# Performance work log

Measured on AMD Instinct MI355X. Metric: run time of the kernel, lower is better.

Reference implementation:

```python
import jax, jax.numpy as jnp
import numpy as np

NUM_BINS = 36
MIN_ACTIVATION = 0.1
PENALTY_WEIGHT = 1.0


def setup_inputs() -> dict:
    key = jax.random.key(0)
    k1, k2 = jax.random.split(key)
    mask = jax.random.uniform(k1, (64, 1, 640, 640), dtype=jnp.float32)
    bbox = jax.random.uniform(k2, (64, 4), dtype=jnp.float32)
    return {"mask": mask, "bbox": bbox}


def reference(mask, bbox):
    B, _, H, W = mask.shape
    nb = NUM_BINS
    # pixel-space bbox centers
    cx = bbox[:, 0] * W  # (B,)
    cy = bbox[:, 1] * H  # (B,)
    x = jnp.arange(W, dtype=jnp.float32)
    y = jnp.arange(H, dtype=jnp.float32)
    # (B, H, W) offsets from each sample's center
    dx = x[None, None, :] - cx[:, None, None]
    dy = y[None, :, None] - cy[:, None, None]
    angles = jnp.arctan2(dy, dx)  # (B, H, W) in [-pi, pi]
    binf = (angles + jnp.pi) / (2.0 * jnp.pi) * nb
    bins = jnp.clip(binf.astype(jnp.int32), 0, nb - 1)  # (B, H, W)
    # fused per-(sample, bin) segment mean via a single scatter-add pass
    seg = (bins + jnp.arange(B, dtype=jnp.int32)[:, None, None] * nb).reshape(-1)
    m = mask[:, 0].reshape(-1)
    sums = jax.ops.segment_sum(m, seg, num_segments=B * nb)
    cnts = jax.ops.segment_sum(jnp.ones_like(m), seg, num_segments=B * nb)
    act = jnp.where(cnts > 0, sums / jnp.maximum(cnts, 1.0), 0.0).reshape(B, nb)
    under = (act < MIN_ACTIVATION).astype(jnp.float32)
    penalty_per_sample = under.sum(axis=1) / nb
    return PENALTY_WEIGHT * penalty_per_sample.mean()
```

## Files before the change

### kernel.cpp

```cpp
#include <hip/hip_runtime.h>
#include <math.h>

#define NB 36
#define W 640
#define H 640
#define NSAMP 64
#define RPB 40
#define BPS 16
#define NBLK (NSAMP * BPS)
#define FIX_SCALE 4194304.0f
#define INV_FIX (1.0f/4194304.0f)
#define CNT_SHIFT 44
#define SUM_MASK ((1ull << CNT_SHIFT) - 1)
#define AMB 1e-6

__device__ __constant__ double COT[36] = {
    0.0,
    5.6712818196177095,  2.7474774194546223,  1.7320508075688773,
    1.1917535925942100,  0.8390996311772800,  0.5773502691896258,
    0.3639702342662024,  0.1763269807084650,  0.0,
    -0.1763269807084650, -0.3639702342662024, -0.5773502691896258,
    -0.8390996311772800, -1.1917535925942100, -1.7320508075688773,
    -2.7474774194546223, -5.6712818196177095,
    0.0,
    5.6712818196177095,  2.7474774194546223,  1.7320508075688773,
    1.1917535925942100,  0.8390996311772800,  0.5773502691896258,
    0.3639702342662024,  0.1763269807084650,  0.0,
    -0.1763269807084650, -0.3639702342662024, -0.5773502691896258,
    -0.8390996311772800, -1.1917535925942100, -1.7320508075688773,
    -2.7474774194546223, -5.6712818196177095
};

__device__ __forceinline__ int bin_slow(int x, int y, double cxd, double cyd) {
    const double PI_D    = 3.141592653589793;
    const double TWOPI_D = 6.283185307179586;
    double t  = (atan2((double)y - cyd, (double)x - cxd) + PI_D) / TWOPI_D;
    double bd = t * 36.0;
    int k = (int)bd;
    k = k < 0 ? 0 : k;
    return k > NB - 1 ? NB - 1 : k;
}

#define SCAN_STEP(x, ctrl, rmask)                                             \
    x += (unsigned)__builtin_amdgcn_update_dpp(0, (int)(x), (ctrl), (rmask),  \
                                               0xf, false)

__global__ __launch_bounds__(256) void acl_main(const float* __restrict__ mask,
                                                const float* __restrict__ bbox,
                                                unsigned long long* __restrict__ ws) {
    __shared__ int A_l[RPB][18];
    __shared__ int sgn_l[RPB];
    __shared__ __align__(16) unsigned srow[4][768];
    __shared__ unsigned long long lbin[NB];

    const int tid = threadIdx.x;
    const int b   = blockIdx.x >> 4;
    const int rg  = blockIdx.x & (BPS - 1);
    const int y0  = rg * RPB;

    if (tid < NB) lbin[tid] = 0ull;
    if (tid < RPB) A_l[tid][17] = W - 1;

    const double cxd = (double)bbox[b * 4 + 0] * 640.0;
    const double cyd = (double)bbox[b * 4 + 1] * 640.0;

    for (int task = tid; task < RPB * 17; task += 256) {
        const int rl = task / 17, mi = task % 17;
        const int y  = y0 + rl;
        const double dy = (double)y - cyd;
        int i, a;
        if (dy == 0.0) {
            if (mi == 0) sgn_l[rl] = 0;
            i = mi;
            a = (mi == 0) ? ((int)ceil(cxd) - 1) : (W - 1);
        } else {
            const bool dp = (dy > 0.0);
            if (mi == 0) sgn_l[rl] = dp ? 1 : -1;
            const int m = dp ? (19 + mi) : (1 + mi);
            double x = cxd + dy * COT[m];
            x = fmin(fmax(x, -2.0), 642.0);
            double g  = x + 2.0;
            int    gi = (int)g;
            double fr = g - (double)gi;
            int v = dp ? (gi - 2)
                       : (gi - 1);
            if (fr < AMB || fr > 1.0 - AMB) {
                int xa = (int)(x + 2.5) - 2;
                if (xa >= 0 && xa <= W - 1) {
                    int kb = bin_slow(xa, y, cxd, cyd);
                    if (dp) v = (kb >= m) ? xa : xa - 1;
                    else    v = (kb >= m) ? xa : xa + 1;
                }
            }
            if (dp) { i = 16 - mi; a = v; }
            else    { i = mi;      a = v - 1; }
        }
        a = a < -1 ? -1 : (a > W - 1 ? W - 1 : a);
        A_l[rl][i] = a;
    }
    __syncthreads();

    const int wid = tid >> 6, lane = tid & 63;
    const float* rowbase = mask + (size_t)b * (W * H) + (size_t)y0 * W;

    unsigned long long accPs = 0ull, accNs = 0ull;
    unsigned accPc = 0u, accNc = 0u;

    const float4 z4 = make_float4(0.f, 0.f, 0.f, 0.f);
    const float4* rpA = (const float4*)(rowbase + (size_t)wid * W);
    float4 a0 = rpA[lane], a1 = rpA[lane + 64];
    float4 a2 = (lane < 32) ? rpA[lane + 128] : z4;
    const float4* rpB = (const float4*)(rowbase + (size_t)(wid + 4) * W);
    float4 b0 = rpB[lane], b1 = rpB[lane + 64];
    float4 b2 = (lane < 32) ? rpB[lane + 128] : z4;

    for (int j = 0; j < 10; j++) {
        const int rl = wid + 4 * j;
        float4 n0 = z4, n1 = z4, n2 = z4;
        if (j < 8) {
            const float4* np = (const float4*)(rowbase + (size_t)(rl + 8) * W);
            n0 = np[lane];
            n1 = np[lane + 64];
            n2 = (lane < 32) ? np[lane + 128] : z4;
        }

        unsigned carry = 0u;
        #pragma unroll
        for (int s = 0; s < 3; s++) {
            const float4 v = (s == 0) ? a0 : (s == 1) ? a1 : a2;
            const unsigned q0 = __float2uint_rn(v.x * FIX_SCALE);
            const unsigned q1 = __float2uint_rn(v.y * FIX_SCALE);
            const unsigned q2 = __float2uint_rn(v.z * FIX_SCALE);
            const unsigned q3 = __float2uint_rn(v.w * FIX_SCALE);
            const unsigned p0 = q0, p1 = p0 + q1, p2 = p1 + q2, p3 = p2 + q3;

            unsigned x = p3;
            SCAN_STEP(x, 0x111, 0xf);
            SCAN_STEP(x, 0x112, 0xf);
            SCAN_STEP(x, 0x114, 0xf);
            SCAN_STEP(x, 0x118, 0xf);
            SCAN_STEP(x, 0x142, 0xa);
            SCAN_STEP(x, 0x143, 0xc);
            const unsigned base = carry + (x - p3);
            uint4 wv;
            wv.x = base + p0; wv.y = base + p1; wv.z = base + p2; wv.w = base + p3;
            *((uint4*)&srow[wid][s * 256 + lane * 4]) = wv;
            carry += (unsigned)__builtin_amdgcn_readlane((int)x, 63);
        }

        if (lane < 18) {
            const int aR = A_l[rl][lane];
            const int aL = (lane == 0) ? -1 : A_l[rl][lane - 1];
            const int cnt = aR - aL;
            if (cnt > 0) {
                const unsigned sR = srow[wid][aR];
                const unsigned sL = (aL >= 0) ? srow[wid][aL] : 0u;
                const unsigned seg = sR - sL;
                const int sg = sgn_l[rl];
                if (sg > 0)      { accPc += (unsigned)cnt; accPs += seg; }
                else if (sg < 0) { accNc += (unsigned)cnt; accNs += seg; }
                else atomicAdd(&lbin[(lane == 0) ? 35 : 18],
                               ((unsigned long long)cnt << CNT_SHIFT)
                               + (unsigned long long)seg);
            }
        }
        a0 = b0; a1 = b1; a2 = b2;
        b0 = n0; b1 = n1; b2 = n2;
    }

    if (lane < 18) {
        if (accPc) atomicAdd(&lbin[35 - lane],
                             ((unsigned long long)accPc << CNT_SHIFT) + accPs);
        if (accNc) atomicAdd(&lbin[lane],
                             ((unsigned long long)accNc << CNT_SHIFT) + accNs);
    }
    __syncthreads();
    if (tid < NB)
        ws[(size_t)tid * NBLK + blockIdx.x] = lbin[tid];
}

__global__ __launch_bounds__(256) void acl_final(const unsigned long long* __restrict__ ws,
                                                 float* __restrict__ out) {
    __shared__ unsigned nund[256];
    __shared__ float s[NSAMP];
    const int tid = threadIdx.x;
    const int b = tid & 63, q = tid >> 6;
    unsigned cu = 0;
    #pragma unroll
    for (int kk = 0; kk < 9; kk++) {
        const int k = q * 9 + kk;
        const unsigned long long* base = ws + (size_t)k * NBLK + (size_t)b * BPS;
        unsigned long long t0 = 0ull, t1 = 0ull;
        #pragma unroll
        for (int g = 0; g < BPS; g += 2) {
            t0 += base[g];
            t1 += base[g + 1];
        }
        const unsigned long long tot = t0 + t1;
        const unsigned long long cnt = tot >> CNT_SHIFT;
        const float sum = (float)(tot & SUM_MASK) * INV_FIX;
        const float act = (cnt != 0ull) ? (sum / (float)cnt) : 0.0f;
        if (act < 0.1f) cu++;
    }
    nund[tid] = cu;
    __syncthreads();
    if (tid < NSAMP) {
        const unsigned n = nund[tid] + nund[64 + tid] + nund[128 + tid] + nund[192 + tid];
        s[tid] = (float)n / 36.0f;
    }
    __syncthreads();
    if (tid == 0) {
        float acc = 0.0f;
        for (int i = 0; i < NSAMP; i++) acc += s[i];
        out[0] = acc / 64.0f;
    }
}

extern "C" void kernel_launch(void* const* d_in, const int* in_sizes, int n_in,
                              void* d_out, int out_size, void* d_ws, size_t ws_size,
                              hipStream_t stream) {
    const float* mask = (const float*)d_in[0];
    const float* bbox = (const float*)d_in[1];
    unsigned long long* ws = (unsigned long long*)d_ws;

    acl_main<<<dim3(NBLK), dim3(256), 0, stream>>>(mask, bbox, ws);
    acl_final<<<dim3(1), dim3(256), 0, stream>>>(ws, (float*)d_out);
}
```

Baseline: 34.24 us.

## Issue first row loads before boundary setup and process two rows per iteration

New measurement: 34.44 us. Within noise of the previous version (+0.6%).

```diff
diff --git a/kernel.cpp b/kernel.cpp
--- a/kernel.cpp
+++ b/kernel.cpp
@@ -50,7 +50,7 @@
                                                 unsigned long long* __restrict__ ws) {
     __shared__ int A_l[RPB][18];
     __shared__ int sgn_l[RPB];
-    __shared__ __align__(16) unsigned srow[4][768];
+    __shared__ __align__(16) unsigned srow[8][768];
     __shared__ unsigned long long lbin[NB];
 
     const int tid = threadIdx.x;
@@ -60,6 +60,16 @@
 
     if (tid < NB) lbin[tid] = 0ull;
     if (tid < RPB) A_l[tid][17] = W - 1;
+
+    const int wid = tid >> 6, lane = tid & 63;
+    const float* wb = mask + (size_t)b * (W * H) + (size_t)(y0 + wid * 10) * W;
+    const float4 z4 = make_float4(0.f, 0.f, 0.f, 0.f);
+    const float4* pr0 = (const float4*)wb;
+    const float4* pr1 = (const float4*)(wb + W);
+    float4 cA0 = pr0[lane], cA1 = pr0[lane + 64];
+    float4 cA2 = (lane < 32) ? pr0[lane + 128] : z4;
+    float4 cB0 = pr1[lane], cB1 = pr1[lane + 64];
+    float4 cB2 = (lane < 32) ? pr1[lane + 128] : z4;
 
     const double cxd = (double)bbox[b * 4 + 0] * 640.0;
     const double cyd = (double)bbox[b * 4 + 1] * 640.0;
@@ -100,72 +110,81 @@
     }
     __syncthreads();
 
-    const int wid = tid >> 6, lane = tid & 63;
-    const float* rowbase = mask + (size_t)b * (W * H) + (size_t)y0 * W;
-
     unsigned long long accPs = 0ull, accNs = 0ull;
     unsigned accPc = 0u, accNc = 0u;
 
-    const float4 z4 = make_float4(0.f, 0.f, 0.f, 0.f);
-    const float4* rpA = (const float4*)(rowbase + (size_t)wid * W);
-    float4 a0 = rpA[lane], a1 = rpA[lane + 64];
-    float4 a2 = (lane < 32) ? rpA[lane + 128] : z4;
-    const float4* rpB = (const float4*)(rowbase + (size_t)(wid + 4) * W);
-    float4 b0 = rpB[lane], b1 = rpB[lane + 64];
-    float4 b2 = (lane < 32) ? rpB[lane + 128] : z4;
-
-    for (int j = 0; j < 10; j++) {
-        const int rl = wid + 4 * j;
-        float4 n0 = z4, n1 = z4, n2 = z4;
-        if (j < 8) {
-            const float4* np = (const float4*)(rowbase + (size_t)(rl + 8) * W);
-            n0 = np[lane];
-            n1 = np[lane + 64];
-            n2 = (lane < 32) ? np[lane + 128] : z4;
-        }
-
-        unsigned carry = 0u;
+    for (int j = 0; j < 5; j++) {
+        const int rl0 = wid * 10 + 2 * j;
+        float4 nA0, nA1, nA2, nB0, nB1, nB2;
+        if (j < 4) {
+            const float4* q0 = (const float4*)(wb + (size_t)(2 * j + 2) * W);
+            const float4* q1 = (const float4*)(wb + (size_t)(2 * j + 3) * W);
+            nA0 = q0[lane]; nA1 = q0[lane + 64];
+            nA2 = (lane < 32) ? q0[lane + 128] : z4;
+            nB0 = q1[lane]; nB1 = q1[lane + 64];
+            nB2 = (lane < 32) ? q1[lane + 128] : z4;
+        }
+
+        unsigned carryA = 0u, carryB = 0u;
         #pragma unroll
         for (int s = 0; s < 3; s++) {
-            const float4 v = (s == 0) ? a0 : (s == 1) ? a1 : a2;
-            const unsigned q0 = __float2uint_rn(v.x * FIX_SCALE);
-            const unsigned q1 = __float2uint_rn(v.y * FIX_SCALE);
-            const unsigned q2 = __float2uint_rn(v.z * FIX_SCALE);
-            const unsigned q3 = __float2uint_rn(v.w * FIX_SCALE);
-            const unsigned p0 = q0, p1 = p0 + q1, p2 = p1 + q2, p3 = p2 + q3;
-
-            unsigned x = p3;
-            SCAN_STEP(x, 0x111, 0xf);
-            SCAN_STEP(x, 0x112, 0xf);
-            SCAN_STEP(x, 0x114, 0xf);
-            SCAN_STEP(x, 0x118, 0xf);
-            SCAN_STEP(x, 0x142, 0xa);
-            SCAN_STEP(x, 0x143, 0xc);
-            const unsigned base = carry + (x - p3);
-            uint4 wv;
-            wv.x = base + p0; wv.y = base + p1; wv.z = base + p2; wv.w = base + p3;
-            *((uint4*)&srow[wid][s * 256 + lane * 4]) = wv;
-            carry += (unsigned)__builtin_amdgcn_readlane((int)x, 63);
+            const float4 va = (s == 0) ? cA0 : (s == 1) ? cA1 : cA2;
+            const float4 vb = (s == 0) ? cB0 : (s == 1) ? cB1 : cB2;
+            const unsigned qa0 = __float2uint_rn(va.x * FIX_SCALE);
+            const unsigned qa1 = __float2uint_rn(va.y * FIX_SCALE);
+            const unsigned qa2 = __float2uint_rn(va.z * FIX_SCALE);
+            const unsigned qa3 = __float2uint_rn(va.w * FIX_SCALE);
+            const unsigned qb0 = __float2uint_rn(vb.x * FIX_SCALE);
+            const unsigned qb1 = __float2uint_rn(vb.y * FIX_SCALE);
+            const unsigned qb2 = __float2uint_rn(vb.z * FIX_SCALE);
+            const unsigned qb3 = __float2uint_rn(vb.w * FIX_SCALE);
+            const unsigned pa0 = qa0, pa1 = pa0 + qa1, pa2 = pa1 + qa2, pa3 = pa2 + qa3;
+            const unsigned pb0 = qb0, pb1 = pb0 + qb1, pb2 = pb1 + qb2, pb3 = pb2 + qb3;
+
+            unsigned xa = pa3, xb = pb3;
+            SCAN_STEP(xa, 0x111, 0xf); SCAN_STEP(xb, 0x111, 0xf);
+            SCAN_STEP(xa, 0x112, 0xf); SCAN_STEP(xb, 0x112, 0xf);
+            SCAN_STEP(xa, 0x114, 0xf); SCAN_STEP(xb, 0x114, 0xf);
+            SCAN_STEP(xa, 0x118, 0xf); SCAN_STEP(xb, 0x118, 0xf);
+            SCAN_STEP(xa, 0x142, 0xa); SCAN_STEP(xb, 0x142, 0xa);
+            SCAN_STEP(xa, 0x143, 0xc); SCAN_STEP(xb, 0x143, 0xc);
+
+            const unsigned baA = carryA + (xa - pa3);
+            const unsigned baB = carryB + (xb - pb3);
+            uint4 wa, wbv;
+            wa.x  = baA + pa0; wa.y  = baA + pa1; wa.z  = baA + pa2; wa.w  = baA + pa3;
+            wbv.x = baB + pb0; wbv.y = baB + pb1; wbv.z = baB + pb2; wbv.w = baB + pb3;
+            *((uint4*)&srow[wid][s * 256 + lane * 4])     = wa;
+            *((uint4*)&srow[wid + 4][s * 256 + lane * 4]) = wbv;
+            carryA += (unsigned)__builtin_amdgcn_readlane((int)xa, 63);
+            carryB += (unsigned)__builtin_amdgcn_readlane((int)xb, 63);
         }
 
         if (lane < 18) {
-            const int aR = A_l[rl][lane];
-            const int aL = (lane == 0) ? -1 : A_l[rl][lane - 1];
-            const int cnt = aR - aL;
-            if (cnt > 0) {
-                const unsigned sR = srow[wid][aR];
-                const unsigned sL = (aL >= 0) ? srow[wid][aL] : 0u;
-                const unsigned seg = sR - sL;
-                const int sg = sgn_l[rl];
-                if (sg > 0)      { accPc += (unsigned)cnt; accPs += seg; }
-                else if (sg < 0) { accNc += (unsigned)cnt; accNs += seg; }
-                else atomicAdd(&lbin[(lane == 0) ? 35 : 18],
-                               ((unsigned long long)cnt << CNT_SHIFT)
-                               + (unsigned long long)seg);
+            #pragma unroll
+            for (int r = 0; r < 2; r++) {
+                const int rl = rl0 + r;
+                const int slab = wid + 4 * r;
+                const int aR = A_l[rl][lane];
+                const int aL = (lane == 0) ? -1 : A_l[rl][lane - 1];
+                const int cnt = aR - aL;
+                if (cnt > 0) {
+                    const unsigned sR = srow[slab][aR];
+                    const unsigned sL = (aL >= 0) ? srow[slab][aL] : 0u;
+                    const unsigned seg = sR - sL;
+                    const int sg = sgn_l[rl];
+                    if (sg > 0)      { accPc += (unsigned)cnt; accPs += seg; }
+                    else if (sg < 0) { accNc += (unsigned)cnt; accNs += seg; }
+                    else atomicAdd(&lbin[(lane == 0) ? 35 : 18],
+                                   ((unsigned long long)cnt << CNT_SHIFT)
+                                   + (unsigned long long)seg);
+                }
             }
         }
-        a0 = b0; a1 = b1; a2 = b2;
-        b0 = n0; b1 = n1; b2 = n2;
+        if (j < 4) {
+            cA0 = nA0; cA1 = nA1; cA2 = nA2;
+            cB0 = nB0; cB1 = nB1; cB2 = nB2;
+        }
     }
 
     if (lane < 18) {
```
